# Kernel tuning notes

Measured on AMD Instinct MI355X. Metric: run time of the kernel, lower is better.

The kernel has to match this reference:

```python
import jax, jax.numpy as jnp
import numpy as np

N_VERTS = 163842  # icosphere level-7 mesh
C = 128
K = 7  # vertex + 6 one-ring neighbors
BN_EPS = 1e-5


def setup_inputs() -> dict:
    key = jax.random.key(0)
    ks = jax.random.split(key, 4)
    x = jax.random.normal(ks[0], (N_VERTS, C), dtype=jnp.float32)
    neigh_orders = jax.random.randint(ks[1], (N_VERTS * K,), 0, N_VERTS, dtype=jnp.int64)
    W1 = jax.random.normal(ks[2], (C, K * C), dtype=jnp.float32) * 0.02
    b1 = jnp.zeros((C,), dtype=jnp.float32)
    gamma1 = jnp.ones((C,), dtype=jnp.float32)
    beta1 = jnp.zeros((C,), dtype=jnp.float32)
    W2 = jax.random.normal(ks[3], (C, K * C), dtype=jnp.float32) * 0.02
    b2 = jnp.zeros((C,), dtype=jnp.float32)
    gamma2 = jnp.ones((C,), dtype=jnp.float32)
    beta2 = jnp.zeros((C,), dtype=jnp.float32)
    return {"x": x, "neigh_orders": neigh_orders, "W1": W1, "b1": b1,
            "gamma1": gamma1, "beta1": beta1, "W2": W2, "b2": b2,
            "gamma2": gamma2, "beta2": beta2}


def _onering_conv(x, neigh_orders, W, b):
    # gather [N*7, C] -> [N, 7*C], then linear
    feat = x[neigh_orders].reshape(x.shape[0], -1)
    return feat @ W.T + b


def _batchnorm(h, gamma, beta):
    # training-mode BatchNorm1d over the vertex (batch) dim, biased variance
    mean = jnp.mean(h, axis=0)
    var = jnp.var(h, axis=0)
    return (h - mean) * jax.lax.rsqrt(var + BN_EPS) * gamma + beta


def _leaky_relu(h):
    return jnp.where(h >= 0, h, 0.2 * h)


def reference(x, neigh_orders, W1, b1, gamma1, beta1, W2, b2, gamma2, beta2):
    h = _onering_conv(x, neigh_orders, W1, b1)
    h = _leaky_relu(_batchnorm(h, gamma1, beta1))
    h = _onering_conv(h, neigh_orders, W2, b2)
    h = _batchnorm(h, gamma2, beta2)
    return _leaky_relu(h + x)  # first_in_block=False -> plain residual
```

## Files before the change

kernel.cpp:

```cpp
#include <hip/hip_runtime.h>

#define NV 163842
#define NC 128
#define KN 7
#define NWELT (NC * KN * NC)
#define BN_EPS 1e-5f
#define NBLK 1281

typedef __attribute__((ext_vector_type(4))) float f32x4;
typedef __attribute__((ext_vector_type(8))) short bf16x8;
typedef __attribute__((ext_vector_type(8))) unsigned short u16x8;

static __device__ __forceinline__ unsigned short f2bf(float f) {
    union { float f; unsigned int u; } v; v.f = f;
    unsigned int r = v.u + 0x7fffu + ((v.u >> 16) & 1u);
    return (unsigned short)(r >> 16);
}
static __device__ __forceinline__ float bf2f(unsigned short s) {
    union { unsigned int u; float f; } v; v.u = ((unsigned int)s) << 16;
    return v.f;
}
static __device__ __forceinline__ void gload_lds16(const void* g, void* l) {
    __builtin_amdgcn_global_load_lds((const __attribute__((address_space(1))) void*)g,
                                     (__attribute__((address_space(3))) void*)l, 16, 0, 0);
}

__global__ void cvt_kernel(const float* __restrict__ x, const float* __restrict__ w1,
                           const float* __restrict__ w2, unsigned short* __restrict__ xbf,
                           unsigned short* __restrict__ w1bf, unsigned short* __restrict__ w2bf)
{
    const int total4 = (NV * NC + 2 * NWELT) / 4;
    for (int i = blockIdx.x * blockDim.x + threadIdx.x; i < total4; i += gridDim.x * blockDim.x) {
        int e = i * 4;
        const float* src; unsigned short* dst;
        if (e < NV * NC)              { src = x  + e;                  dst = xbf  + e; }
        else if (e < NV * NC + NWELT) { src = w1 + (e - NV * NC);      dst = w1bf + (e - NV * NC); }
        else                          { src = w2 + (e - NV * NC - NWELT); dst = w2bf + (e - NV * NC - NWELT); }
        float4 v = *(const float4*)src;
        ushort4 o;
        o.x = f2bf(v.x); o.y = f2bf(v.y); o.z = f2bf(v.z); o.w = f2bf(v.w);
        *(ushort4*)dst = o;
    }
}

__global__ __launch_bounds__(512, 4)
void conv_kernel(const unsigned short* __restrict__ xin,
                 const int* __restrict__ neigh,
                 const unsigned short* __restrict__ wbf,
                 unsigned short* __restrict__ hout,
                 float* __restrict__ psum, float* __restrict__ psq)
{
    __shared__ __align__(16) char smem[65536];

    const int t    = threadIdx.x;
    const int row0 = blockIdx.x * 128;
    const int w    = t >> 6;
    const int lane = t & 63;
    const int lrow = lane & 15;
    const int lgrp = lane >> 4;
    const int wr   = w >> 2;
    const int wc   = w & 3;

    const int sl   = lane & 7;
    const int r3   = lane >> 3;
    const int srcoff = (sl ^ r3) << 4;

    const int rA0 = w * 16 + r3;
    const int g0  = (row0 + rA0     < NV) ? (row0 + rA0)     : (NV - 1);
    const int g1  = (row0 + rA0 + 8 < NV) ? (row0 + rA0 + 8) : (NV - 1);

    int idx0[KN], idx1[KN];
    #pragma unroll
    for (int k = 0; k < KN; ++k) {
        idx0[k] = neigh[g0 * KN + k];
        idx1[k] = neigh[g1 * KN + k];
    }

    const char* xinb = (const char*)xin;
    const char* bsrc0 = (const char*)wbf + (size_t)(w * 16 + r3) * 1792 + srcoff;
    const char* bsrc1 = (const char*)wbf + (size_t)(w * 16 + 8 + r3) * 1792 + srcoff;

    f32x4 acc[4][2];
    #pragma unroll
    for (int mf = 0; mf < 4; ++mf)
        #pragma unroll
        for (int nf = 0; nf < 2; ++nf)
            acc[mf][nf] = (f32x4){0.f, 0.f, 0.f, 0.f};

#define STAGE(c) do {                                                              \
        const int h_ = (c) & 1, k_ = (c) >> 1, bs_ = ((c) & 1) * 32768;            \
        char* lA = smem + bs_ + w * 2048;                                          \
        char* lB = smem + bs_ + 16384 + w * 2048;                                  \
        gload_lds16(xinb + (size_t)idx0[k_] * 256 + h_ * 128 + srcoff, lA);        \
        gload_lds16(xinb + (size_t)idx1[k_] * 256 + h_ * 128 + srcoff, lA + 1024); \
        gload_lds16(bsrc0 + k_ * 256 + h_ * 128, lB);                              \
        gload_lds16(bsrc1 + k_ * 256 + h_ * 128, lB + 1024);                       \
    } while (0)

    STAGE(0);
    asm volatile("s_waitcnt vmcnt(0)" ::: "memory");
    __builtin_amdgcn_s_barrier();
    __builtin_amdgcn_sched_barrier(0);

    #pragma unroll
    for (int c = 0; c < 14; ++c) {
        if (c < 13) STAGE(c + 1);

        const char* Ab = smem + (c & 1) * 32768;
        const char* Bb = Ab + 16384;
        #pragma unroll
        for (int ks = 0; ks < 2; ++ks) {
            const int koff = ks * 64 + lgrp * 16;
            bf16x8 a[4], b[2];
            #pragma unroll
            for (int mf = 0; mf < 4; ++mf) {
                const int arow = wr * 64 + mf * 16 + lrow;
                a[mf] = *(const bf16x8*)(Ab + ((arow * 128 + koff) ^ ((arow & 7) << 4)));
            }
            #pragma unroll
            for (int nf = 0; nf < 2; ++nf) {
                const int bcol = wc * 32 + nf * 16 + lrow;
                b[nf] = *(const bf16x8*)(Bb + ((bcol * 128 + koff) ^ ((bcol & 7) << 4)));
            }
            #pragma unroll
            for (int mf = 0; mf < 4; ++mf) {
                acc[mf][0] = __builtin_amdgcn_mfma_f32_16x16x32_bf16(a[mf], b[0], acc[mf][0], 0, 0, 0);
                acc[mf][1] = __builtin_amdgcn_mfma_f32_16x16x32_bf16(a[mf], b[1], acc[mf][1], 0, 0, 0);
            }
        }

        if (c < 13) {
            asm volatile("s_waitcnt vmcnt(0)" ::: "memory");
            __builtin_amdgcn_sched_barrier(0);
            __builtin_amdgcn_s_barrier();
            __builtin_amdgcn_sched_barrier(0);
        }
    }
#undef STAGE

    float* redsum = (float*)smem;
    float* redsq  = (float*)(smem + 1024);

    #pragma unroll
    for (int nf = 0; nf < 2; ++nf) {
        const int col = wc * 32 + nf * 16 + lrow;
        float sum = 0.f, sq = 0.f;
        #pragma unroll
        for (int mf = 0; mf < 4; ++mf) {
            const int rbase = row0 + wr * 64 + mf * 16 + lgrp * 4;
            #pragma unroll
            for (int r = 0; r < 4; ++r) {
                float v = acc[mf][nf][r];
                const int grow = rbase + r;
                if (grow < NV) {
                    sum += v; sq += v * v;
                    hout[(size_t)grow * NC + col] = f2bf(v);
                }
            }
        }
        sum += __shfl_xor(sum, 16); sum += __shfl_xor(sum, 32);
        sq  += __shfl_xor(sq, 16);  sq  += __shfl_xor(sq, 32);
        if (lgrp == 0) { redsum[wr * 128 + col] = sum; redsq[wr * 128 + col] = sq; }
    }
    __syncthreads();
    if (t < 128) {
        psum[(size_t)blockIdx.x * 128 + t] = redsum[t] + redsum[128 + t];
        psq[(size_t)blockIdx.x * 128 + t]  = redsq[t]  + redsq[128 + t];
    }
}

__global__ void bn_stats_kernel(const float* __restrict__ psum, const float* __restrict__ psq,
                                const float* __restrict__ gamma, const float* __restrict__ beta,
                                float* __restrict__ scale, float* __restrict__ shift)
{
    const int c = blockIdx.x;
    const int t = threadIdx.x;
    float s = 0.f, q = 0.f;
    for (int b = t; b < NBLK; b += 128) {
        s += psum[b * 128 + c];
        q += psq[b * 128 + c];
    }
    #pragma unroll
    for (int o = 1; o < 64; o <<= 1) {
        s += __shfl_xor(s, o);
        q += __shfl_xor(q, o);
    }
    __shared__ float ls[2], lq[2];
    if ((t & 63) == 0) { ls[t >> 6] = s; lq[t >> 6] = q; }
    __syncthreads();
    if (t == 0) {
        const float S = ls[0] + ls[1];
        const float Q = lq[0] + lq[1];
        const float inv  = 1.f / (float)NV;
        const float mean = S * inv;
        const float var  = Q * inv - mean * mean;
        const float sc   = gamma[c] * rsqrtf(var + BN_EPS);
        scale[c] = sc;
        shift[c] = beta[c] - mean * sc;
    }
}

__global__ void bn_apply_kernel(const unsigned short* __restrict__ h, const float* __restrict__ scale,
                                const float* __restrict__ shift, unsigned short* __restrict__ outbf)
{
    __shared__ float ssc[NC], ssh[NC];
    if (threadIdx.x < NC) { ssc[threadIdx.x] = scale[threadIdx.x]; ssh[threadIdx.x] = shift[threadIdx.x]; }
    __syncthreads();
    const int total8 = NV * NC / 8;
    for (int i = blockIdx.x * blockDim.x + threadIdx.x; i < total8; i += gridDim.x * blockDim.x) {
        const int e = i * 8;
        const int c0 = e & (NC - 1);
        u16x8 v = *(const u16x8*)(h + e);
        u16x8 o;
        #pragma unroll
        for (int j = 0; j < 8; ++j) {
            float a = bf2f(v[j]) * ssc[c0 + j] + ssh[c0 + j];
            a = a >= 0.f ? a : 0.2f * a;
            o[j] = f2bf(a);
        }
        *(u16x8*)(outbf + e) = o;
    }
}

__global__ void final_kernel(const unsigned short* __restrict__ h, const float* __restrict__ x,
                             const unsigned short* __restrict__ xb, const int use_bf,
                             const float* __restrict__ scale, const float* __restrict__ shift,
                             float* __restrict__ out)
{
    __shared__ float ssc[NC], ssh[NC];
    if (threadIdx.x < NC) { ssc[threadIdx.x] = scale[threadIdx.x]; ssh[threadIdx.x] = shift[threadIdx.x]; }
    __syncthreads();
    const int total8 = NV * NC / 8;
    for (int i = blockIdx.x * blockDim.x + threadIdx.x; i < total8; i += gridDim.x * blockDim.x) {
        const int e = i * 8;
        const int c0 = e & (NC - 1);
        u16x8 v = *(const u16x8*)(h + e);
        float xv[8];
        if (use_bf) {
            u16x8 xvb = *(const u16x8*)(xb + e);
            #pragma unroll
            for (int j = 0; j < 8; ++j) xv[j] = bf2f(xvb[j]);
        } else {
            float4 x0 = *(const float4*)(x + e);
            float4 x1 = *(const float4*)(x + e + 4);
            xv[0]=x0.x; xv[1]=x0.y; xv[2]=x0.z; xv[3]=x0.w;
            xv[4]=x1.x; xv[5]=x1.y; xv[6]=x1.z; xv[7]=x1.w;
        }
        float ov[8];
        #pragma unroll
        for (int j = 0; j < 8; ++j) {
            float a = bf2f(v[j]) * ssc[c0 + j] + ssh[c0 + j] + xv[j];
            ov[j] = a >= 0.f ? a : 0.2f * a;
        }
        float4 o0 = {ov[0], ov[1], ov[2], ov[3]};
        float4 o1 = {ov[4], ov[5], ov[6], ov[7]};
        *(float4*)(out + e)     = o0;
        *(float4*)(out + e + 4) = o1;
    }
}

extern "C" void kernel_launch(void* const* d_in, const int* in_sizes, int n_in,
                              void* d_out, int out_size, void* d_ws, size_t ws_size,
                              hipStream_t stream)
{
    const float* x      = (const float*)d_in[0];
    const int*   neigh  = (const int*)d_in[1];
    const float* W1     = (const float*)d_in[2];
    const float* gamma1 = (const float*)d_in[4];
    const float* beta1  = (const float*)d_in[5];
    const float* W2     = (const float*)d_in[6];
    const float* gamma2 = (const float*)d_in[8];
    const float* beta2  = (const float*)d_in[9];

    unsigned short* h1pre = (unsigned short*)d_out;
    unsigned short* h1bn  = (unsigned short*)d_out + (size_t)NV * NC;
    float* out = (float*)d_out;

    char* ws = (char*)d_ws;
    size_t off = 0;
    unsigned short* xbf  = (unsigned short*)(ws + off); off += (size_t)NV * NC * 2;
    unsigned short* w1bf = (unsigned short*)(ws + off); off += NWELT * 2;
    unsigned short* w2bf = (unsigned short*)(ws + off); off += NWELT * 2;
    float* psum  = (float*)(ws + off); off += (size_t)NBLK * 128 * 4;
    float* psq   = (float*)(ws + off); off += (size_t)NBLK * 128 * 4;
    float* scale1 = (float*)(ws + off); off += 512;
    float* shift1 = (float*)(ws + off); off += 512;
    float* scale2 = (float*)(ws + off); off += 512;
    float* shift2 = (float*)(ws + off); off += 512;

    const size_t h2_bytes = (size_t)NV * NC * 2;
    unsigned short* h2pre;
    int use_bf;
    if (off + h2_bytes <= ws_size) { h2pre = (unsigned short*)(ws + off); use_bf = 1; }
    else                           { h2pre = xbf;                        use_bf = 0; }

    cvt_kernel<<<2048, 256, 0, stream>>>(x, W1, W2, xbf, w1bf, w2bf);
    conv_kernel<<<NBLK, 512, 0, stream>>>(xbf, neigh, w1bf, h1pre, psum, psq);
    bn_stats_kernel<<<128, 128, 0, stream>>>(psum, psq, gamma1, beta1, scale1, shift1);
    bn_apply_kernel<<<2048, 256, 0, stream>>>(h1pre, scale1, shift1, h1bn);
    conv_kernel<<<NBLK, 512, 0, stream>>>(h1bn, neigh, w2bf, h2pre, psum, psq);
    bn_stats_kernel<<<128, 128, 0, stream>>>(psum, psq, gamma2, beta2, scale2, shift2);
    final_kernel<<<2048, 256, 0, stream>>>(h2pre, x, xbf, use_bf, scale2, shift2, out);
}
```

Measured before the change: 187.1 us.

## Fuse BN1 apply and leaky ReLU into second conv's gather stage

```diff
diff --git a/kernel.cpp b/kernel.cpp
--- a/kernel.cpp
+++ b/kernel.cpp
@@ -23,6 +23,18 @@
 static __device__ __forceinline__ void gload_lds16(const void* g, void* l) {
     __builtin_amdgcn_global_load_lds((const __attribute__((address_space(1))) void*)g,
                                      (__attribute__((address_space(3))) void*)l, 16, 0, 0);
+}
+static __device__ __forceinline__ unsigned int bn_pair(unsigned int u, float s0, float t0,
+                                                       float s1, float t1) {
+    float lo = __uint_as_float(u << 16);
+    float hi = __uint_as_float(u & 0xffff0000u);
+    float a = fmaf(lo, s0, t0);
+    float b = fmaf(hi, s1, t1);
+    a = fmaxf(a, 0.f) + 0.2f * fminf(a, 0.f);
+    b = fmaxf(b, 0.f) + 0.2f * fminf(b, 0.f);
+    unsigned int r;
+    asm("v_cvt_pk_bf16_f32 %0, %1, %2" : "=v"(r) : "v"(a), "v"(b));
+    return r;
 }
 
 __global__ void cvt_kernel(const float* __restrict__ x, const float* __restrict__ w1,
@@ -137,6 +149,174 @@
         }
     }
 #undef STAGE
+
+    float* redsum = (float*)smem;
+    float* redsq  = (float*)(smem + 1024);
+
+    #pragma unroll
+    for (int nf = 0; nf < 2; ++nf) {
+        const int col = wc * 32 + nf * 16 + lrow;
+        float sum = 0.f, sq = 0.f;
+        #pragma unroll
+        for (int mf = 0; mf < 4; ++mf) {
+            const int rbase = row0 + wr * 64 + mf * 16 + lgrp * 4;
+            #pragma unroll
+            for (int r = 0; r < 4; ++r) {
+                float v = acc[mf][nf][r];
+                const int grow = rbase + r;
+                if (grow < NV) {
+                    sum += v; sq += v * v;
+                    hout[(size_t)grow * NC + col] = f2bf(v);
+                }
+            }
+        }
+        sum += __shfl_xor(sum, 16); sum += __shfl_xor(sum, 32);
+        sq  += __shfl_xor(sq, 16);  sq  += __shfl_xor(sq, 32);
+        if (lgrp == 0) { redsum[wr * 128 + col] = sum; redsq[wr * 128 + col] = sq; }
+    }
+    __syncthreads();
+    if (t < 128) {
+        psum[(size_t)blockIdx.x * 128 + t] = redsum[t] + redsum[128 + t];
+        psq[(size_t)blockIdx.x * 128 + t]  = redsq[t]  + redsq[128 + t];
+    }
+}
+
+__global__ __launch_bounds__(512, 4)
+void conv_fused_kernel(const unsigned short* __restrict__ xin,
+                 const int* __restrict__ neigh,
+                 const unsigned short* __restrict__ wbf,
+                 const float* __restrict__ scale, const float* __restrict__ shift,
+                 unsigned short* __restrict__ hout,
+                 float* __restrict__ psum, float* __restrict__ psq)
+{
+    __shared__ __align__(16) char smem[65536];
+
+    const int t    = threadIdx.x;
+    const int row0 = blockIdx.x * 128;
+    const int w    = t >> 6;
+    const int lane = t & 63;
+    const int lrow = lane & 15;
+    const int lgrp = lane >> 4;
+    const int wr   = w >> 2;
+    const int wc   = w & 3;
+
+    const int sl   = lane & 7;
+    const int r3   = lane >> 3;
+    const int srcoff = (sl ^ r3) << 4;
+
+    const int rA0 = w * 16 + r3;
+    const int g0  = (row0 + rA0     < NV) ? (row0 + rA0)     : (NV - 1);
+    const int g1  = (row0 + rA0 + 8 < NV) ? (row0 + rA0 + 8) : (NV - 1);
+
+    int idx0[KN], idx1[KN];
+    #pragma unroll
+    for (int k = 0; k < KN; ++k) {
+        idx0[k] = neigh[g0 * KN + k];
+        idx1[k] = neigh[g1 * KN + k];
+    }
+
+    const int cb = (sl ^ r3) * 8;
+    float sc[2][8], sh[2][8];
+    #pragma unroll
+    for (int j = 0; j < 8; ++j) {
+        sc[0][j] = scale[cb + j];       sh[0][j] = shift[cb + j];
+        sc[1][j] = scale[64 + cb + j];  sh[1][j] = shift[64 + cb + j];
+    }
+
+    const char* xinb = (const char*)xin;
+    const char* bsrc0 = (const char*)wbf + (size_t)(w * 16 + r3) * 1792 + srcoff;
+    const char* bsrc1 = (const char*)wbf + (size_t)(w * 16 + 8 + r3) * 1792 + srcoff;
+
+    f32x4 acc[4][2];
+    #pragma unroll
+    for (int mf = 0; mf < 4; ++mf)
+        #pragma unroll
+        for (int nf = 0; nf < 2; ++nf)
+            acc[mf][nf] = (f32x4){0.f, 0.f, 0.f, 0.f};
+
+    {
+        uint4 sa0 = *(const uint4*)(xinb + (size_t)idx0[0] * 256 + srcoff);
+        uint4 sa1 = *(const uint4*)(xinb + (size_t)idx1[0] * 256 + srcoff);
+        gload_lds16(bsrc0, smem + 16384 + w * 2048);
+        gload_lds16(bsrc1, smem + 16384 + w * 2048 + 1024);
+        asm volatile("s_waitcnt vmcnt(2)" ::: "memory");
+        __builtin_amdgcn_sched_barrier(0);
+        char* lA = smem + w * 2048 + lane * 16;
+        uint4 o0, o1;
+        o0.x = bn_pair(sa0.x, sc[0][0], sh[0][0], sc[0][1], sh[0][1]);
+        o0.y = bn_pair(sa0.y, sc[0][2], sh[0][2], sc[0][3], sh[0][3]);
+        o0.z = bn_pair(sa0.z, sc[0][4], sh[0][4], sc[0][5], sh[0][5]);
+        o0.w = bn_pair(sa0.w, sc[0][6], sh[0][6], sc[0][7], sh[0][7]);
+        o1.x = bn_pair(sa1.x, sc[0][0], sh[0][0], sc[0][1], sh[0][1]);
+        o1.y = bn_pair(sa1.y, sc[0][2], sh[0][2], sc[0][3], sh[0][3]);
+        o1.z = bn_pair(sa1.z, sc[0][4], sh[0][4], sc[0][5], sh[0][5]);
+        o1.w = bn_pair(sa1.w, sc[0][6], sh[0][6], sc[0][7], sh[0][7]);
+        *(uint4*)lA          = o0;
+        *(uint4*)(lA + 1024) = o1;
+        asm volatile("s_waitcnt vmcnt(0)" ::: "memory");
+        asm volatile("s_waitcnt lgkmcnt(0)" ::: "memory");
+        __builtin_amdgcn_sched_barrier(0);
+        __builtin_amdgcn_s_barrier();
+        __builtin_amdgcn_sched_barrier(0);
+    }
+
+    #pragma unroll
+    for (int c = 0; c < 14; ++c) {
+        uint4 sa0, sa1;
+        if (c < 13) {
+            const int k_ = (c + 1) >> 1, h_ = (c + 1) & 1, bs_ = ((c + 1) & 1) * 32768;
+            sa0 = *(const uint4*)(xinb + (size_t)idx0[k_] * 256 + h_ * 128 + srcoff);
+            sa1 = *(const uint4*)(xinb + (size_t)idx1[k_] * 256 + h_ * 128 + srcoff);
+            gload_lds16(bsrc0 + k_ * 256 + h_ * 128, smem + bs_ + 16384 + w * 2048);
+            gload_lds16(bsrc1 + k_ * 256 + h_ * 128, smem + bs_ + 16384 + w * 2048 + 1024);
+        }
+
+        const char* Ab = smem + (c & 1) * 32768;
+        const char* Bb = Ab + 16384;
+        #pragma unroll
+        for (int ks = 0; ks < 2; ++ks) {
+            const int koff = ks * 64 + lgrp * 16;
+            bf16x8 a[4], b[2];
+            #pragma unroll
+            for (int mf = 0; mf < 4; ++mf) {
+                const int arow = wr * 64 + mf * 16 + lrow;
+                a[mf] = *(const bf16x8*)(Ab + ((arow * 128 + koff) ^ ((arow & 7) << 4)));
+            }
+            #pragma unroll
+            for (int nf = 0; nf < 2; ++nf) {
+                const int bcol = wc * 32 + nf * 16 + lrow;
+                b[nf] = *(const bf16x8*)(Bb + ((bcol * 128 + koff) ^ ((bcol & 7) << 4)));
+            }
+            #pragma unroll
+            for (int mf = 0; mf < 4; ++mf) {
+                acc[mf][0] = __builtin_amdgcn_mfma_f32_16x16x32_bf16(a[mf], b[0], acc[mf][0], 0, 0, 0);
+                acc[mf][1] = __builtin_amdgcn_mfma_f32_16x16x32_bf16(a[mf], b[1], acc[mf][1], 0, 0, 0);
+            }
+        }
+
+        if (c < 13) {
+            const int hn = (c + 1) & 1, bs_ = ((c + 1) & 1) * 32768;
+            asm volatile("s_waitcnt vmcnt(2)" ::: "memory");
+            __builtin_amdgcn_sched_barrier(0);
+            char* lA = smem + bs_ + w * 2048 + lane * 16;
+            uint4 o0, o1;
+            o0.x = bn_pair(sa0.x, sc[hn][0], sh[hn][0], sc[hn][1], sh[hn][1]);
+            o0.y = bn_pair(sa0.y, sc[hn][2], sh[hn][2], sc[hn][3], sh[hn][3]);
+            o0.z = bn_pair(sa0.z, sc[hn][4], sh[hn][4], sc[hn][5], sh[hn][5]);
+            o0.w = bn_pair(sa0.w, sc[hn][6], sh[hn][6], sc[hn][7], sh[hn][7]);
+            o1.x = bn_pair(sa1.x, sc[hn][0], sh[hn][0], sc[hn][1], sh[hn][1]);
+            o1.y = bn_pair(sa1.y, sc[hn][2], sh[hn][2], sc[hn][3], sh[hn][3]);
+            o1.z = bn_pair(sa1.z, sc[hn][4], sh[hn][4], sc[hn][5], sh[hn][5]);
+            o1.w = bn_pair(sa1.w, sc[hn][6], sh[hn][6], sc[hn][7], sh[hn][7]);
+            *(uint4*)lA          = o0;
+            *(uint4*)(lA + 1024) = o1;
+            asm volatile("s_waitcnt vmcnt(0)" ::: "memory");
+            asm volatile("s_waitcnt lgkmcnt(0)" ::: "memory");
+            __builtin_amdgcn_sched_barrier(0);
+            __builtin_amdgcn_s_barrier();
+            __builtin_amdgcn_sched_barrier(0);
+        }
+    }
 
     float* redsum = (float*)smem;
     float* redsq  = (float*)(smem + 1024);
@@ -200,28 +380,6 @@
     }
 }
 
-__global__ void bn_apply_kernel(const unsigned short* __restrict__ h, const float* __restrict__ scale,
-                                const float* __restrict__ shift, unsigned short* __restrict__ outbf)
-{
-    __shared__ float ssc[NC], ssh[NC];
-    if (threadIdx.x < NC) { ssc[threadIdx.x] = scale[threadIdx.x]; ssh[threadIdx.x] = shift[threadIdx.x]; }
-    __syncthreads();
-    const int total8 = NV * NC / 8;
-    for (int i = blockIdx.x * blockDim.x + threadIdx.x; i < total8; i += gridDim.x * blockDim.x) {
-        const int e = i * 8;
-        const int c0 = e & (NC - 1);
-        u16x8 v = *(const u16x8*)(h + e);
-        u16x8 o;
-        #pragma unroll
-        for (int j = 0; j < 8; ++j) {
-            float a = bf2f(v[j]) * ssc[c0 + j] + ssh[c0 + j];
-            a = a >= 0.f ? a : 0.2f * a;
-            o[j] = f2bf(a);
-        }
-        *(u16x8*)(outbf + e) = o;
-    }
-}
-
 __global__ void final_kernel(const unsigned short* __restrict__ h, const float* __restrict__ x,
                              const unsigned short* __restrict__ xb, const int use_bf,
                              const float* __restrict__ scale, const float* __restrict__ shift,
@@ -273,7 +431,6 @@
     const float* beta2  = (const float*)d_in[9];
 
     unsigned short* h1pre = (unsigned short*)d_out;
-    unsigned short* h1bn  = (unsigned short*)d_out + (size_t)NV * NC;
     float* out = (float*)d_out;
 
     char* ws = (char*)d_ws;
@@ -297,8 +454,7 @@
     cvt_kernel<<<2048, 256, 0, stream>>>(x, W1, W2, xbf, w1bf, w2bf);
     conv_kernel<<<NBLK, 512, 0, stream>>>(xbf, neigh, w1bf, h1pre, psum, psq);
     bn_stats_kernel<<<128, 128, 0, stream>>>(psum, psq, gamma1, beta1, scale1, shift1);
-    bn_apply_kernel<<<2048, 256, 0, stream>>>(h1pre, scale1, shift1, h1bn);
-    conv_kernel<<<NBLK, 512, 0, stream>>>(h1bn, neigh, w2bf, h2pre, psum, psq);
+    conv_fused_kernel<<<NBLK, 512, 0, stream>>>(h1pre, neigh, w2bf, scale1, shift1, h2pre, psum, psq);
     bn_stats_kernel<<<128, 128, 0, stream>>>(psum, psq, gamma2, beta2, scale2, shift2);
     final_kernel<<<2048, 256, 0, stream>>>(h2pre, x, xbf, use_bf, scale2, shift2, out);
 }
```

Measured after the change: 184.6 us (median of 2 runs). Within noise of the previous version (-1.3%).
